# Optimization experiments

Hardware: AMD Instinct MI355X
Metric: run time of the kernel (lower is better)

The kernel has to match this reference:

```python
import jax, jax.numpy as jnp
import numpy as np

N = 50000          # num nodes
E = 800000         # num edges
H, C = 2, 64       # heads, per-head channels (hidden_dim=64)
IN_DIM = 128
EDGE_DIM = 32
NEG_SLOPE = 0.2


def setup_inputs() -> dict:
    key = jax.random.key(0)
    ks = jax.random.split(key, 20)
    s = 0.05
    inp = {
        'x': jax.random.normal(ks[0], (N, IN_DIM), jnp.float32),
        'edge_index': jax.random.randint(ks[1], (2, E), 0, N, jnp.int64),
        'edge_attr': jax.random.normal(ks[2], (E, EDGE_DIM), jnp.float32),
    }
    k = 3
    for l in range(3):
        inp[f'Wl{l}'] = jax.random.normal(ks[k], (IN_DIM, H * C), jnp.float32) * s; k += 1
        inp[f'Wr{l}'] = jax.random.normal(ks[k], (IN_DIM, H * C), jnp.float32) * s; k += 1
        inp[f'We{l}'] = jax.random.normal(ks[k], (EDGE_DIM, H * C), jnp.float32) * s; k += 1
        inp[f'att{l}'] = jax.random.normal(ks[k], (H, C), jnp.float32) * s; k += 1
        inp[f'b{l}'] = jnp.zeros((H * C,), jnp.float32)
    return inp


def gatv2_layer(x, src, dst, edge_attr, Wl, Wr, We, att, b):
    # PyG GATv2Conv (concat=True, share_weights=False):
    #   e_ij = att . LeakyReLU(Wl x_j + Wr x_i + We edge_ij)
    #   alpha = softmax_j over neighborhood of dst i; out_i = sum_j alpha_ij * (Wl x_j)
    xl = (x @ Wl).reshape(-1, H, C)              # [N,H,C] source transform
    xr = (x @ Wr).reshape(-1, H, C)              # [N,H,C] target transform
    ea = (edge_attr @ We).reshape(-1, H, C)      # [E,H,C]
    xj = xl[src]                                 # [E,H,C] gather source
    e = jax.nn.leaky_relu(xj + xr[dst] + ea, NEG_SLOPE)
    logits = jnp.einsum('ehc,hc->eh', e, att)    # [E,H]
    # segment softmax over dst neighborhoods
    m = jax.ops.segment_max(logits, dst, num_segments=N)  # [N,H]
    m = jnp.where(jnp.isfinite(m), m, 0.0)
    ex = jnp.exp(logits - m[dst])
    denom = jax.ops.segment_sum(ex, dst, num_segments=N)  # [N,H]
    alpha = ex / (denom[dst] + 1e-16)            # [E,H]
    out = jax.ops.segment_sum(alpha[:, :, None] * xj, dst, num_segments=N)  # [N,H,C]
    return out.reshape(-1, H * C) + b


def reference(x, edge_index, edge_attr,
              Wl0, Wr0, We0, att0, b0,
              Wl1, Wr1, We1, att1, b1,
              Wl2, Wr2, We2, att2, b2):
    src, dst = edge_index[0], edge_index[1]
    h = gatv2_layer(x, src, dst, edge_attr, Wl0, Wr0, We0, att0, b0)
    h = jax.nn.relu(h)
    h = gatv2_layer(h, src, dst, edge_attr, Wl1, Wr1, We1, att1, b1)
    h = jax.nn.relu(h)
    h = gatv2_layer(h, src, dst, edge_attr, Wl2, Wr2, We2, att2, b2)
    return h
```

## Files before the change

### kernel.cpp

```cpp
#include <hip/hip_runtime.h>

typedef unsigned int u32;
typedef unsigned short u16;
typedef __attribute__((ext_vector_type(8))) short bf16x8;
typedef __attribute__((ext_vector_type(4))) float f32x4;

__device__ __forceinline__ u16 f2b(float f){
  u32 x = __float_as_uint(f);
  u32 r = (x + 0x7fffu + ((x >> 16) & 1u)) >> 16;
  return (u16)r;
}
__device__ __forceinline__ float b2f(u16 h){ return __uint_as_float((u32)h << 16); }
__device__ __forceinline__ float bl(u32 u){ return __uint_as_float(u << 16); }
__device__ __forceinline__ float bh(u32 u){ return __uint_as_float(u & 0xffff0000u); }


__global__ void k_detect(const u32* __restrict__ ei, int n, u32* __restrict__ flag){
  int t = blockIdx.x * blockDim.x + threadIdx.x;
  u32 v = 0;
  if (t < n) v = ei[2 * t + 1];
  unsigned long long b = __ballot(v != 0u);
  if ((threadIdx.x & 63) == 0 && b) atomicOr(flag, 1u);
}

__global__ void k_convhist(const int* __restrict__ ei, int* __restrict__ src, int* __restrict__ dst,
                           int* __restrict__ deg, const float* __restrict__ eattr,
                           u16* __restrict__ ea2, int E, const u32* __restrict__ flag){
  int e = blockIdx.x * blockDim.x + threadIdx.x;
  if (e >= E) return;
  bool is64 = (*flag == 0u);
  int s, d;
  if (is64){ s = ei[2 * e]; d = ei[2 * (E + e)]; }
  else     { s = ei[e];     d = ei[E + e]; }
  src[e] = s; dst[e] = d;
  atomicAdd(&deg[d], 1);
  const float4* srow = (const float4*)(eattr + (size_t)e * 32);
  u32 pk[16];
  #pragma unroll
  for (int i = 0; i < 8; i++){
    float4 v = srow[i];
    pk[2*i]   = (u32)f2b(v.x) | ((u32)f2b(v.y) << 16);
    pk[2*i+1] = (u32)f2b(v.z) | ((u32)f2b(v.w) << 16);
  }
  uint4* drow = (uint4*)(ea2 + (size_t)e * 32);
  drow[0] = make_uint4(pk[0], pk[1], pk[2], pk[3]);
  drow[1] = make_uint4(pk[4], pk[5], pk[6], pk[7]);
  drow[2] = make_uint4(pk[8], pk[9], pk[10], pk[11]);
  drow[3] = make_uint4(pk[12], pk[13], pk[14], pk[15]);
}

__global__ __launch_bounds__(256) void k_scan1(const int* __restrict__ deg, int* __restrict__ bsum, int n,
                                               int* __restrict__ ssrc, int* __restrict__ sdst,
                                               u16* __restrict__ ea2s_pad, int E){
  int b = blockIdx.x, t = threadIdx.x, lane = t & 63, wv = t >> 6;
  if (b == 0){
    if (t < 64){ ssrc[E + t] = 0; sdst[E + t] = 0; }
    ((uint4*)ea2s_pad)[t] = make_uint4(0, 0, 0, 0);
  }
  int i0 = b * 1024 + t * 4;
  int4 v = make_int4(0,0,0,0);
  if (i0 + 3 < n) v = *(const int4*)(deg + i0);
  else { if (i0 < n) v.x = deg[i0]; if (i0+1 < n) v.y = deg[i0+1]; if (i0+2 < n) v.z = deg[i0+2]; }
  int s = v.x + v.y + v.z + v.w;
  #pragma unroll
  for (int off = 1; off < 64; off <<= 1) s += __shfl_xor(s, off);
  __shared__ int ws[4];
  if (lane == 0) ws[wv] = s;
  __syncthreads();
  if (t == 0) bsum[b] = ws[0] + ws[1] + ws[2] + ws[3];
}

__global__ __launch_bounds__(1024) void k_scan2(int* __restrict__ bsum, int nb, int* __restrict__ segN){
  int t = threadIdx.x, lane = t & 63, w = t >> 6;
  int v = (t < nb) ? bsum[t] : 0;
  int x = v;
  #pragma unroll
  for (int off = 1; off < 64; off <<= 1){
    int y = __shfl_up(x, off);
    if (lane >= off) x += y;
  }
  __shared__ int wsum[16];
  if (lane == 63) wsum[w] = x;
  __syncthreads();
  if (w == 0 && lane < 16){
    int sv = wsum[lane];
    #pragma unroll
    for (int off = 1; off < 16; off <<= 1){
      int y = __shfl_up(sv, off);
      if (lane >= off) sv += y;
    }
    wsum[lane] = sv;
  }
  __syncthreads();
  int woff = (w > 0) ? wsum[w - 1] : 0;
  if (t < nb) bsum[t] = woff + x - v;
  if (t == 0) *segN = wsum[15];
}

__global__ __launch_bounds__(256) void k_scan3(const int* __restrict__ deg, const int* __restrict__ bsum,
                                               int* __restrict__ seg, int n){
  int b = blockIdx.x, t = threadIdx.x, lane = t & 63, wv = t >> 6;
  int i0 = b * 1024 + t * 4;
  int4 v = make_int4(0,0,0,0);
  if (i0 + 3 < n) v = *(const int4*)(deg + i0);
  else { if (i0 < n) v.x = deg[i0]; if (i0+1 < n) v.y = deg[i0+1]; if (i0+2 < n) v.z = deg[i0+2]; }
  int s = v.x + v.y + v.z + v.w;
  int x = s;
  #pragma unroll
  for (int off = 1; off < 64; off <<= 1){
    int y = __shfl_up(x, off);
    if (lane >= off) x += y;
  }
  __shared__ int ws[4];
  if (lane == 63) ws[wv] = x;
  __syncthreads();
  int woff = 0;
  #pragma unroll
  for (int k = 0; k < 4; k++) if (k < wv) woff += ws[k];
  int base = bsum[b] + woff + (x - s);
  if (i0 < n)     seg[i0]     = base;
  if (i0+1 < n)   seg[i0+1]   = base + v.x;
  if (i0+2 < n)   seg[i0+2]   = base + v.x + v.y;
  if (i0+3 < n)   seg[i0+3]   = base + v.x + v.y + v.z;
}

__global__ void k_scatter(const int* __restrict__ src, const int* __restrict__ dst,
                          const int* __restrict__ seg, int* __restrict__ cur,
                          int* __restrict__ ssrc, int* __restrict__ sdst,
                          int* __restrict__ seid, int E){
  int e = blockIdx.x * blockDim.x + threadIdx.x;
  if (e >= E) return;
  int d = dst[e];
  int pos = seg[d] + atomicAdd(&cur[d], 1);
  ssrc[pos] = src[e];
  sdst[pos] = d;
  seid[pos] = e;
}

__global__ void k_sortb(const int* __restrict__ seid, const u16* __restrict__ ea2o,
                        u16* __restrict__ ea2s, int E){
  int t = blockIdx.x * blockDim.x + threadIdx.x;
  int e = t >> 2, j = t & 3;
  if (e >= E) return;
  int eid = seid[e];
  uint4 v = *(const uint4*)(ea2o + (size_t)eid * 32 + j * 8);
  *(uint4*)(ea2s + (size_t)e * 32 + j * 8) = v;
}

__global__ __launch_bounds__(256) void k_prepw(
    const float* __restrict__ W0, const float* __restrict__ W1, const float* __restrict__ W2,
    const float* __restrict__ W3, const float* __restrict__ W4, const float* __restrict__ W5,
    u16* __restrict__ WtH, u16* __restrict__ WtL)
{
  int mat = blockIdx.z;
  const float* W = (mat == 0) ? W0 : (mat == 1) ? W1 : (mat == 2) ? W2 :
                   (mat == 3) ? W3 : (mat == 4) ? W4 : W5;
  __shared__ float tile[32][33];
  int kt = blockIdx.x * 32, ct = blockIdx.y * 32;
  int tr = threadIdx.x & 31, ti = threadIdx.x >> 5;
  #pragma unroll
  for (int j = 0; j < 4; j++){
    int kk = ti + 8 * j;
    tile[kk][tr] = W[(size_t)(kt + kk) * 128 + ct + tr];
  }
  __syncthreads();
  #pragma unroll
  for (int j = 0; j < 4; j++){
    int cc = ti + 8 * j;
    float v = tile[tr][cc];
    u16 hi = f2b(v);
    u16 lo = f2b(v - b2f(hi));
    size_t o = (size_t)mat * 16384 + (size_t)(ct + cc) * 128 + kt + tr;
    WtH[o] = hi;
    WtL[o] = lo;
  }
}

__global__ __launch_bounds__(256) void k_gemm2(
    const float* __restrict__ A,
    const u16* __restrict__ WtH, const u16* __restrict__ WtL,
    u16* __restrict__ xlb, u16* __restrict__ xrb, int nrows)
{
  __shared__ u16 sAH[64][32], sAL[64][32];
  __shared__ u16 sWH[128][32], sWL[128][32];
  int t = threadIdx.x, wv = t >> 6, lane = t & 63;
  int col = lane & 15, kg = lane >> 4;
  int r0 = blockIdx.x * 64;
  int mat = blockIdx.y;
  const u16* WHb = WtH + (size_t)mat * 16384;
  const u16* WLb = WtL + (size_t)mat * 16384;

  f32x4 acc[4][2];
  #pragma unroll
  for (int m = 0; m < 4; m++)
    #pragma unroll
    for (int n = 0; n < 2; n++)
      acc[m][n] = (f32x4){0.f, 0.f, 0.f, 0.f};

  int ar = t >> 2, ak = (t & 3) << 3;
  int wc = t >> 1, wk = (t & 1) << 4;

  for (int kh = 0; kh < 4; kh++){
    __syncthreads();
    {
      int gr = r0 + ar;
      const float* ap = A + (size_t)gr * 128 + kh * 32 + ak;
      float4 va = {0,0,0,0}, vb = {0,0,0,0};
      if (gr < nrows){ va = *(const float4*)ap; vb = *(const float4*)(ap + 4); }
      float fv[8] = { va.x, va.y, va.z, va.w, vb.x, vb.y, vb.z, vb.w };
      u32 hp[4], lp[4];
      #pragma unroll
      for (int i = 0; i < 4; i++){
        u16 h0 = f2b(fv[2*i]),   h1 = f2b(fv[2*i+1]);
        u16 l0 = f2b(fv[2*i]   - b2f(h0));
        u16 l1 = f2b(fv[2*i+1] - b2f(h1));
        hp[i] = (u32)h0 | ((u32)h1 << 16);
        lp[i] = (u32)l0 | ((u32)l1 << 16);
      }
      *(uint4*)&sAH[ar][ak] = make_uint4(hp[0], hp[1], hp[2], hp[3]);
      *(uint4*)&sAL[ar][ak] = make_uint4(lp[0], lp[1], lp[2], lp[3]);
    }
    {
      const u16* gh = WHb + (size_t)wc * 128 + kh * 32 + wk;
      const u16* gl = WLb + (size_t)wc * 128 + kh * 32 + wk;
      uint4 h0 = *(const uint4*)gh, h1 = *(const uint4*)(gh + 8);
      uint4 l0 = *(const uint4*)gl, l1 = *(const uint4*)(gl + 8);
      *(uint4*)&sWH[wc][wk]     = h0; *(uint4*)&sWH[wc][wk + 8] = h1;
      *(uint4*)&sWL[wc][wk]     = l0; *(uint4*)&sWL[wc][wk + 8] = l1;
    }
    __syncthreads();
    bf16x8 bhi0 = *(const bf16x8*)&sWH[wv*32 + col]     [kg*8];
    bf16x8 bhi1 = *(const bf16x8*)&sWH[wv*32 + 16 + col][kg*8];
    bf16x8 blo0 = *(const bf16x8*)&sWL[wv*32 + col]     [kg*8];
    bf16x8 blo1 = *(const bf16x8*)&sWL[wv*32 + 16 + col][kg*8];
    #pragma unroll
    for (int m = 0; m < 4; m++){
      bf16x8 ahv = *(const bf16x8*)&sAH[m*16 + col][kg*8];
      bf16x8 alv = *(const bf16x8*)&sAL[m*16 + col][kg*8];
      acc[m][0] = __builtin_amdgcn_mfma_f32_16x16x32_bf16(ahv, bhi0, acc[m][0], 0, 0, 0);
      acc[m][0] = __builtin_amdgcn_mfma_f32_16x16x32_bf16(alv, bhi0, acc[m][0], 0, 0, 0);
      acc[m][0] = __builtin_amdgcn_mfma_f32_16x16x32_bf16(ahv, blo0, acc[m][0], 0, 0, 0);
      acc[m][1] = __builtin_amdgcn_mfma_f32_16x16x32_bf16(ahv, bhi1, acc[m][1], 0, 0, 0);
      acc[m][1] = __builtin_amdgcn_mfma_f32_16x16x32_bf16(alv, bhi1, acc[m][1], 0, 0, 0);
      acc[m][1] = __builtin_amdgcn_mfma_f32_16x16x32_bf16(ahv, blo1, acc[m][1], 0, 0, 0);
    }
  }
  u16* ob = mat ? xrb : xlb;
  #pragma unroll
  for (int m = 0; m < 4; m++){
    #pragma unroll
    for (int n = 0; n < 2; n++){
      #pragma unroll
      for (int r = 0; r < 4; r++){
        int row = r0 + m*16 + kg*4 + r;
        int c   = wv*32 + n*16 + col;
        if (row < nrows) ob[(size_t)row * 128 + c] = f2b(acc[m][n][r]);
      }
    }
  }
}

__global__ __launch_bounds__(256) void k_edge(
    const int* __restrict__ ssrc, const int* __restrict__ sdst,
    const u16* __restrict__ ea2s,
    const u16* __restrict__ xlb, const u16* __restrict__ xrb,
    const float* __restrict__ We, const float* __restrict__ att,
    float2* __restrict__ pr2, int ntiles, int E)
{
  __shared__ float sD[4][16][132];
  int wv = threadIdx.x >> 6, lane = threadIdx.x & 63;
  int col = lane & 15, kg = lane >> 4;
  int er = lane >> 2, q = lane & 3;

  bf16x8 bw[8];
  #pragma unroll
  for (int c = 0; c < 8; c++)
    #pragma unroll
    for (int j = 0; j < 8; j++)
      bw[c][j] = (short)f2b(We[(kg * 8 + j) * 128 + c * 16 + col]);
  u32 attp[16];
  #pragma unroll
  for (int i = 0; i < 16; i++)
    attp[i] = (u32)f2b(att[q * 32 + 2*i]) | ((u32)f2b(att[q * 32 + 2*i + 1]) << 16);

  int nw = gridDim.x * 4;
  int t = blockIdx.x * 4 + wv;
  if (t >= ntiles) return;

  int e0 = t * 16;
  int p = e0 + er;
  bf16x8 aA = *(const bf16x8*)(ea2s + (size_t)(e0 + col) * 32 + kg * 8);
  int snA = ssrc[p], dnA = sdst[p];
  const u16* xjA = xlb + (size_t)snA * 128 + q * 32;
  uint4 jA0 = ((const uint4*)xjA)[0], jA1 = ((const uint4*)xjA)[1],
        jA2 = ((const uint4*)xjA)[2], jA3 = ((const uint4*)xjA)[3];

  int tB = t + nw;
  int tBc = (tB < ntiles) ? tB : t;
  int eB = tBc * 16;
  int pB = eB + er;
  bf16x8 aB = *(const bf16x8*)(ea2s + (size_t)(eB + col) * 32 + kg * 8);
  int snB = ssrc[pB], dnB = sdst[pB];
  const u16* xjB = xlb + (size_t)snB * 128 + q * 32;
  uint4 jB0 = ((const uint4*)xjB)[0], jB1 = ((const uint4*)xjB)[1],
        jB2 = ((const uint4*)xjB)[2], jB3 = ((const uint4*)xjB)[3];

  while (true){
    const u16* xip = xrb + (size_t)dnA * 128 + q * 32;
    uint4 i0 = ((const uint4*)xip)[0], i1 = ((const uint4*)xip)[1],
          i2 = ((const uint4*)xip)[2], i3 = ((const uint4*)xip)[3];

    int tC = t + 2 * nw;
    int tCc = (tC < ntiles) ? tC : t;
    int eC = tCc * 16;
    int pC = eC + er;
    bf16x8 aC = *(const bf16x8*)(ea2s + (size_t)(eC + col) * 32 + kg * 8);
    int snC = ssrc[pC], dnC = sdst[pC];
    const u16* xjC = xlb + (size_t)snC * 128 + q * 32;
    uint4 jC0 = ((const uint4*)xjC)[0], jC1 = ((const uint4*)xjC)[1],
          jC2 = ((const uint4*)xjC)[2], jC3 = ((const uint4*)xjC)[3];

    #pragma unroll
    for (int c = 0; c < 8; c++){
      f32x4 d = __builtin_amdgcn_mfma_f32_16x16x32_bf16(aA, bw[c], (f32x4){0.f,0.f,0.f,0.f}, 0, 0, 0);
      #pragma unroll
      for (int r = 0; r < 4; r++)
        sD[wv][kg * 4 + r][c * 16 + col] = d[r];
    }

    const float* drow = &sD[wv][er][q * 32];
    float acc = 0.f;
#define EPK(KO, JQ, IQ) { \
    float4 d0 = *(const float4*)(drow + KO*8); \
    float4 d1 = *(const float4*)(drow + KO*8 + 4); \
    float v; u32 jw, iw, aw; \
    jw = JQ.x; iw = IQ.x; aw = attp[KO*4+0]; \
    v = d0.x + bl(jw) + bl(iw); v = fmaxf(v, 0.2f*v); acc = fmaf(v, bl(aw), acc); \
    v = d0.y + bh(jw) + bh(iw); v = fmaxf(v, 0.2f*v); acc = fmaf(v, bh(aw), acc); \
    jw = JQ.y; iw = IQ.y; aw = attp[KO*4+1]; \
    v = d0.z + bl(jw) + bl(iw); v = fmaxf(v, 0.2f*v); acc = fmaf(v, bl(aw), acc); \
    v = d0.w + bh(jw) + bh(iw); v = fmaxf(v, 0.2f*v); acc = fmaf(v, bh(aw), acc); \
    jw = JQ.z; iw = IQ.z; aw = attp[KO*4+2]; \
    v = d1.x + bl(jw) + bl(iw); v = fmaxf(v, 0.2f*v); acc = fmaf(v, bl(aw), acc); \
    v = d1.y + bh(jw) + bh(iw); v = fmaxf(v, 0.2f*v); acc = fmaf(v, bh(aw), acc); \
    jw = JQ.w; iw = IQ.w; aw = attp[KO*4+3]; \
    v = d1.z + bl(jw) + bl(iw); v = fmaxf(v, 0.2f*v); acc = fmaf(v, bl(aw), acc); \
    v = d1.w + bh(jw) + bh(iw); v = fmaxf(v, 0.2f*v); acc = fmaf(v, bh(aw), acc); }
    EPK(0, jA0, i0) EPK(1, jA1, i1) EPK(2, jA2, i2) EPK(3, jA3, i3)
#undef EPK
    acc += __shfl_xor(acc, 1);
    float other = __shfl_xor(acc, 2);
    if (q == 0 && p < E){
      pr2[p] = make_float2(__expf(fminf(acc, 80.f)), __expf(fminf(other, 80.f)));
    }
    int t2 = t + nw;
    if (t2 >= ntiles) break;
    t = t2; p = pB;
    aA = aB; dnA = dnB;
    jA0 = jB0; jA1 = jB1; jA2 = jB2; jA3 = jB3;
    aB = aC; dnB = dnC; pB = pC;
    jB0 = jC0; jB1 = jC1; jB2 = jC2; jB3 = jC3;
  }
}

template<int RELU>
__global__ __launch_bounds__(256) void k_seg2(
    const int* __restrict__ seg, const int* __restrict__ ssrc,
    const float2* __restrict__ pr2,
    const u16* __restrict__ xlb, const float* __restrict__ bias,
    float* __restrict__ out, int N)
{
  int wid  = blockIdx.x * 4 + (threadIdx.x >> 6);
  int lane = threadIdx.x & 63;
  if (wid >= N) return;
  int eg = lane >> 4, cb = lane & 15, c0 = cb * 8;
  int hsel = cb >> 3;

  int p0 = seg[wid], p1 = seg[wid + 1];
  float s = 0.f;
  float o0 = 0.f, o1 = 0.f, o2 = 0.f, o3 = 0.f, o4 = 0.f, o5 = 0.f, o6 = 0.f, o7 = 0.f;

  if (p0 < p1){
#define LDB(PP, QV, XV) { \
    int ii = PP + eg; ii = (ii < p1) ? ii : (p1 - 1); \
    int sn = ssrc[ii]; \
    QV = pr2[ii]; \
    XV = *(const uint4*)(xlb + (size_t)sn * 128 + c0); }
    float2 qa; uint4 xa;
    LDB(p0, qa, xa)
    int p = p0;
    while (true){
      int pn = p + 4;
      bool more = pn < p1;
      int pc = more ? pn : p;
      float2 qb; uint4 xb;
      LDB(pc, qb, xb)
      float e = hsel ? qa.y : qa.x;
      if (p + eg >= p1) e = 0.f;
      s += e;
      o0 = fmaf(e, bl(xa.x), o0); o1 = fmaf(e, bh(xa.x), o1);
      o2 = fmaf(e, bl(xa.y), o2); o3 = fmaf(e, bh(xa.y), o3);
      o4 = fmaf(e, bl(xa.z), o4); o5 = fmaf(e, bh(xa.z), o5);
      o6 = fmaf(e, bl(xa.w), o6); o7 = fmaf(e, bh(xa.w), o7);
      if (!more) break;
      p = pn; qa = qb; xa = xb;
    }
#undef LDB
  }
  s  += __shfl_xor(s, 16);  s  += __shfl_xor(s, 32);
  o0 += __shfl_xor(o0, 16); o0 += __shfl_xor(o0, 32);
  o1 += __shfl_xor(o1, 16); o1 += __shfl_xor(o1, 32);
  o2 += __shfl_xor(o2, 16); o2 += __shfl_xor(o2, 32);
  o3 += __shfl_xor(o3, 16); o3 += __shfl_xor(o3, 32);
  o4 += __shfl_xor(o4, 16); o4 += __shfl_xor(o4, 32);
  o5 += __shfl_xor(o5, 16); o5 += __shfl_xor(o5, 32);
  o6 += __shfl_xor(o6, 16); o6 += __shfl_xor(o6, 32);
  o7 += __shfl_xor(o7, 16); o7 += __shfl_xor(o7, 32);

  if (eg == 0){
    float inv = 1.0f / (s + 1e-16f);
    float4 b0 = *(const float4*)(bias + c0);
    float4 b1 = *(const float4*)(bias + c0 + 4);
    float r0 = fmaf(o0, inv, b0.x), r1 = fmaf(o1, inv, b0.y);
    float r2 = fmaf(o2, inv, b0.z), r3 = fmaf(o3, inv, b0.w);
    float r4 = fmaf(o4, inv, b1.x), r5 = fmaf(o5, inv, b1.y);
    float r6 = fmaf(o6, inv, b1.z), r7 = fmaf(o7, inv, b1.w);
    if (RELU){
      r0 = fmaxf(r0, 0.f); r1 = fmaxf(r1, 0.f); r2 = fmaxf(r2, 0.f); r3 = fmaxf(r3, 0.f);
      r4 = fmaxf(r4, 0.f); r5 = fmaxf(r5, 0.f); r6 = fmaxf(r6, 0.f); r7 = fmaxf(r7, 0.f);
    }
    *(float4*)(out + (size_t)wid * 128 + c0)     = make_float4(r0, r1, r2, r3);
    *(float4*)(out + (size_t)wid * 128 + c0 + 4) = make_float4(r4, r5, r6, r7);
  }
}

extern "C" void kernel_launch(void* const* d_in, const int* in_sizes, int n_in,
                              void* d_out, int out_size, void* d_ws, size_t ws_size,
                              hipStream_t stream)
{
  const float* x     = (const float*)d_in[0];
  const int*   ei    = (const int*)  d_in[1];
  const float* eattr = (const float*)d_in[2];
  const float* Wp[3][5];
  for (int l = 0; l < 3; l++)
    for (int j = 0; j < 5; j++)
      Wp[l][j] = (const float*)d_in[3 + l * 5 + j];

  int N = in_sizes[0] / 128;
  int E = in_sizes[2] / 32;

  char* w = (char*)d_ws;
  auto alloc = [&](size_t bytes) -> char* {
    char* p = w; w += (bytes + 255) & ~(size_t)255; return p;
  };
  float* xr   = (float*)alloc((size_t)N * 128 * 4);
  u16*   xlb  = (u16*)  alloc((size_t)N * 128 * 2);
  u16*   xrb  = (u16*)  alloc((size_t)N * 128 * 2);
  u16*   ea2o = (u16*)  alloc((size_t)E * 32 * 2);
  u16*   ea2s = (u16*)  alloc((size_t)(E + 64) * 32 * 2);
  float2* prb = (float2*)alloc((size_t)E * 8);
  u16*   WtH  = (u16*)  alloc((size_t)6 * 16384 * 2);
  u16*   WtL  = (u16*)  alloc((size_t)6 * 16384 * 2);
  int* srcA   = (int*)alloc((size_t)E * 4);
  int* dstA   = (int*)alloc((size_t)E * 4);
  int* ssrc   = (int*)alloc((size_t)(E + 64) * 4);
  int* sdst   = (int*)alloc((size_t)(E + 64) * 4);
  int* seid   = (int*)alloc((size_t)E * 4);
  int* seg    = (int*)alloc((size_t)(N + 1) * 4);
  int* bsum   = (int*)alloc(1024 * 4);
  char* zbase = alloc((size_t)N * 4);      int* deg  = (int*)zbase;
  char* zcur  = alloc((size_t)N * 4);      int* cur  = (int*)zcur;
  char* zflag = alloc(256);                u32* flag = (u32*)zflag;
  size_t zspan = (size_t)(zflag + 256 - zbase);

  hipMemsetAsync(zbase, 0, zspan, stream);

  int ndet = (E < 16384) ? E : 16384;
  k_detect<<<(ndet + 255) / 256, 256, 0, stream>>>((const u32*)ei, ndet, flag);
  int gE = (E + 255) / 256;
  k_convhist<<<gE, 256, 0, stream>>>(ei, srcA, dstA, deg, eattr, ea2o, E, flag);
  int nb = (N + 1023) / 1024;
  k_scan1<<<nb, 256, 0, stream>>>(deg, bsum, N, ssrc, sdst, ea2s + (size_t)E * 32, E);
  k_scan2<<<1, 1024, 0, stream>>>(bsum, nb, seg + N);
  k_scan3<<<nb, 256, 0, stream>>>(deg, bsum, seg, N);
  k_scatter<<<gE, 256, 0, stream>>>(srcA, dstA, seg, cur, ssrc, sdst, seid, E);
  k_sortb<<<(E * 4 + 255) / 256, 256, 0, stream>>>(seid, ea2o, ea2s, E);
  dim3 gp(4, 4, 6);
  k_prepw<<<gp, 256, 0, stream>>>(Wp[0][0], Wp[0][1], Wp[1][0], Wp[1][1], Wp[2][0], Wp[2][1], WtH, WtL);

  int gS = (N + 3) / 4;
  int ntiles = (E + 15) / 16;
  int gEdge = (ntiles + 3) / 4; if (gEdge > 2048) gEdge = 2048;
  dim3 gG2((N + 63) / 64, 2);

  const float* hin = x;
  for (int l = 0; l < 3; l++){
    k_gemm2<<<gG2, 256, 0, stream>>>(hin, WtH + (size_t)l * 2 * 16384, WtL + (size_t)l * 2 * 16384, xlb, xrb, N);
    k_edge<<<gEdge, 256, 0, stream>>>(ssrc, sdst, ea2s, xlb, xrb, Wp[l][2], Wp[l][3], prb, ntiles, E);
    float* outp = (l == 2) ? (float*)d_out : xr;
    if (l == 2) k_seg2<0><<<gS, 256, 0, stream>>>(seg, ssrc, prb, xlb, Wp[l][4], outp, N);
    else        k_seg2<1><<<gS, 256, 0, stream>>>(seg, ssrc, prb, xlb, Wp[l][4], outp, N);
    hin = xr;
  }
}
```

Measured before the change: 471.2 us.

## Fuse edge-attr bf16 conversion into sort gather, remap edge blocks, deepen segment prefetch

```diff
diff --git a/kernel.cpp b/kernel.cpp
--- a/kernel.cpp
+++ b/kernel.cpp
@@ -24,8 +24,7 @@
 }
 
 __global__ void k_convhist(const int* __restrict__ ei, int* __restrict__ src, int* __restrict__ dst,
-                           int* __restrict__ deg, const float* __restrict__ eattr,
-                           u16* __restrict__ ea2, int E, const u32* __restrict__ flag){
+                           int* __restrict__ deg, int E, const u32* __restrict__ flag){
   int e = blockIdx.x * blockDim.x + threadIdx.x;
   if (e >= E) return;
   bool is64 = (*flag == 0u);
@@ -34,19 +33,6 @@
   else     { s = ei[e];     d = ei[E + e]; }
   src[e] = s; dst[e] = d;
   atomicAdd(&deg[d], 1);
-  const float4* srow = (const float4*)(eattr + (size_t)e * 32);
-  u32 pk[16];
-  #pragma unroll
-  for (int i = 0; i < 8; i++){
-    float4 v = srow[i];
-    pk[2*i]   = (u32)f2b(v.x) | ((u32)f2b(v.y) << 16);
-    pk[2*i+1] = (u32)f2b(v.z) | ((u32)f2b(v.w) << 16);
-  }
-  uint4* drow = (uint4*)(ea2 + (size_t)e * 32);
-  drow[0] = make_uint4(pk[0], pk[1], pk[2], pk[3]);
-  drow[1] = make_uint4(pk[4], pk[5], pk[6], pk[7]);
-  drow[2] = make_uint4(pk[8], pk[9], pk[10], pk[11]);
-  drow[3] = make_uint4(pk[12], pk[13], pk[14], pk[15]);
 }
 
 __global__ __launch_bounds__(256) void k_scan1(const int* __restrict__ deg, int* __restrict__ bsum, int n,
@@ -137,14 +123,16 @@
   seid[pos] = e;
 }
 
-__global__ void k_sortb(const int* __restrict__ seid, const u16* __restrict__ ea2o,
+__global__ void k_sortb(const int* __restrict__ seid, const float* __restrict__ eattr,
                         u16* __restrict__ ea2s, int E){
   int t = blockIdx.x * blockDim.x + threadIdx.x;
-  int e = t >> 2, j = t & 3;
+  int e = t >> 3, j = t & 7;
   if (e >= E) return;
   int eid = seid[e];
-  uint4 v = *(const uint4*)(ea2o + (size_t)eid * 32 + j * 8);
-  *(uint4*)(ea2s + (size_t)e * 32 + j * 8) = v;
+  float4 v = *(const float4*)(eattr + (size_t)eid * 32 + j * 4);
+  u32 p0 = (u32)f2b(v.x) | ((u32)f2b(v.y) << 16);
+  u32 p1 = (u32)f2b(v.z) | ((u32)f2b(v.w) << 16);
+  *(uint2*)(ea2s + (size_t)e * 32 + j * 4) = make_uint2(p0, p1);
 }
 
 __global__ __launch_bounds__(256) void k_prepw(
@@ -284,7 +272,12 @@
     attp[i] = (u32)f2b(att[q * 32 + 2*i]) | ((u32)f2b(att[q * 32 + 2*i + 1]) << 16);
 
   int nw = gridDim.x * 4;
-  int t = blockIdx.x * 4 + wv;
+  int bid = blockIdx.x;
+  if ((gridDim.x & 7) == 0){
+    int cpx = gridDim.x >> 3;
+    bid = (bid & 7) * cpx + (bid >> 3);
+  }
+  int t = bid * 4 + wv;
   if (t >= ntiles) return;
 
   int e0 = t * 16;
@@ -386,15 +379,16 @@
     int sn = ssrc[ii]; \
     QV = pr2[ii]; \
     XV = *(const uint4*)(xlb + (size_t)sn * 128 + c0); }
+    int p = p0;
     float2 qa; uint4 xa;
-    LDB(p0, qa, xa)
-    int p = p0;
+    LDB(p, qa, xa)
+    int pBb = p + 4; int pBc = (pBb < p1) ? pBb : p;
+    float2 qb; uint4 xb;
+    LDB(pBc, qb, xb)
     while (true){
-      int pn = p + 4;
-      bool more = pn < p1;
-      int pc = more ? pn : p;
-      float2 qb; uint4 xb;
-      LDB(pc, qb, xb)
+      int pCb = p + 8; int pCc = (pCb < p1) ? pCb : p;
+      float2 qc; uint4 xc;
+      LDB(pCc, qc, xc)
       float e = hsel ? qa.y : qa.x;
       if (p + eg >= p1) e = 0.f;
       s += e;
@@ -402,8 +396,10 @@
       o2 = fmaf(e, bl(xa.y), o2); o3 = fmaf(e, bh(xa.y), o3);
       o4 = fmaf(e, bl(xa.z), o4); o5 = fmaf(e, bh(xa.z), o5);
       o6 = fmaf(e, bl(xa.w), o6); o7 = fmaf(e, bh(xa.w), o7);
-      if (!more) break;
-      p = pn; qa = qb; xa = xb;
+      if (p + 4 >= p1) break;
+      p += 4;
+      qa = qb; xa = xb;
+      qb = qc; xb = xc;
     }
 #undef LDB
   }
@@ -456,7 +452,6 @@
   float* xr   = (float*)alloc((size_t)N * 128 * 4);
   u16*   xlb  = (u16*)  alloc((size_t)N * 128 * 2);
   u16*   xrb  = (u16*)  alloc((size_t)N * 128 * 2);
-  u16*   ea2o = (u16*)  alloc((size_t)E * 32 * 2);
   u16*   ea2s = (u16*)  alloc((size_t)(E + 64) * 32 * 2);
   float2* prb = (float2*)alloc((size_t)E * 8);
   u16*   WtH  = (u16*)  alloc((size_t)6 * 16384 * 2);
@@ -478,13 +473,13 @@
   int ndet = (E < 16384) ? E : 16384;
   k_detect<<<(ndet + 255) / 256, 256, 0, stream>>>((const u32*)ei, ndet, flag);
   int gE = (E + 255) / 256;
-  k_convhist<<<gE, 256, 0, stream>>>(ei, srcA, dstA, deg, eattr, ea2o, E, flag);
+  k_convhist<<<gE, 256, 0, stream>>>(ei, srcA, dstA, deg, E, flag);
   int nb = (N + 1023) / 1024;
   k_scan1<<<nb, 256, 0, stream>>>(deg, bsum, N, ssrc, sdst, ea2s + (size_t)E * 32, E);
   k_scan2<<<1, 1024, 0, stream>>>(bsum, nb, seg + N);
   k_scan3<<<nb, 256, 0, stream>>>(deg, bsum, seg, N);
   k_scatter<<<gE, 256, 0, stream>>>(srcA, dstA, seg, cur, ssrc, sdst, seid, E);
-  k_sortb<<<(E * 4 + 255) / 256, 256, 0, stream>>>(seid, ea2o, ea2s, E);
+  k_sortb<<<(E * 8 + 255) / 256, 256, 0, stream>>>(seid, eattr, ea2s, E);
   dim3 gp(4, 4, 6);
   k_prepw<<<gp, 256, 0, stream>>>(Wp[0][0], Wp[0][1], Wp[1][0], Wp[1][1], Wp[2][0], Wp[2][1], WtH, WtL);
 
```

After: 471.1 us. Within noise of the previous version (-0.0%).
